# Kernel tuning notes

Hardware: AMD Instinct MI355X
Metric: run time of the kernel (lower is better)

Reference implementation:

```python
import jax, jax.numpy as jnp
import numpy as np

B = 131072
N = 19  # num_features, fixed by the hard-coded 19x19 correlation matrix


def _make_corr():
    corr = np.eye(N, dtype=np.float32)
    for i, j, v in [(0, 1, 0.9088), (2, 3, 0.7964), (2, 4, 0.6972),
                    (2, 9, -0.6945), (4, 9, -0.6679)]:
        corr[i, j] = corr[j, i] = v
    return jnp.asarray(corr)


def setup_inputs() -> dict:
    key = jax.random.key(0)
    ks = jax.random.split(key, 9)
    bound = 1.0 / np.sqrt(N)  # torch nn.Linear default init range

    def linear_params(k):
        kw, kb = jax.random.split(k)
        W = jax.random.uniform(kw, (N, N), jnp.float32, -bound, bound)
        b = jax.random.uniform(kb, (N,), jnp.float32, -bound, bound)
        return W, b

    Wq, bq = linear_params(ks[0])
    Wk, bk = linear_params(ks[1])
    Wv, bv = linear_params(ks[2])
    Wo, bo = linear_params(ks[3])
    features = jax.random.normal(ks[4], (B, N), jnp.float32)
    return {
        "features": features,
        "Wq": Wq, "bq": bq,
        "Wk": Wk, "bk": bk,
        "Wv": Wv, "bv": bv,
        "Wo": Wo, "bo": bo,
        "corr": _make_corr(),
        "temperature": jnp.array(1.0, jnp.float32),
    }


def reference(features, Wq, bq, Wk, bk, Wv, bv, Wo, bo, corr, temperature):
    # Projections (torch Linear: x @ W.T + b)
    Q = features @ Wq.T + bq  # [B, N]
    K = features @ Wk.T + bk  # [B, N]
    V = features @ Wv.T + bv  # [B, N]

    # Outer-product scores: bmm(Q[:, :, None], K[:, None, :]) -> [B, N, N]
    scores = Q[:, :, None] * K[:, None, :]

    # correlation_weight = (corr @ K.T).T = K @ corr.T ; mean over features -> [B]
    cw_mean = (K @ corr.T).mean(axis=-1)
    scores = scores * cw_mean[:, None, None]

    attention = jax.nn.softmax(scores / temperature, axis=-1)  # [B, N, N]

    # Elementwise combine (attention * V broadcast over the query axis)
    attended = attention * V[:, None, :]  # [B, N, N]

    output = attended @ Wo.T + bo  # [B, N, N]

    # Residual: features broadcast over the query axis
    return features[:, None, :] + output  # [B, N, N]
```

## Files before the change

kernel.cpp:

```cpp
#include <hip/hip_runtime.h>

#define B_TOTAL 131072
#define N 19
#define BB 13
#define ROWS (BB * N)
#define NPAD 20
#define OUT_PER_G (BB * N * N)

__global__ void cga_prep(const float* __restrict__ corr, float* __restrict__ c) {
    int t = threadIdx.x;
    if (t < N) {
        float s = 0.f;
#pragma unroll
        for (int i = 0; i < N; ++i) s += corr[i * N + t];
        c[t] = s * (1.0f / N);
    }
}

__global__ void __launch_bounds__(256) cga_kernel(
    const float* __restrict__ feats,
    const float* __restrict__ Wq, const float* __restrict__ bq,
    const float* __restrict__ Wk, const float* __restrict__ bk,
    const float* __restrict__ Wv, const float* __restrict__ bv,
    const float* __restrict__ Wo, const float* __restrict__ bo,
    const float* __restrict__ temp,
    const float* __restrict__ c,
    float* __restrict__ out)
{
    __shared__ __align__(16) float feat_s[BB * NPAD];
    __shared__ __align__(16) float k_s[BB * NPAD];
    __shared__ __align__(16) float v_s[BB * NPAD];
    __shared__ __align__(16) float out_s[OUT_PER_G];

    const int t = threadIdx.x;
    const int bl = t / N;
    const int i  = t - bl * N;
    const bool active = (t < ROWS);

    float wq[N], wk[N], wv[N];
    float bqv = 0.f, bkv = 0.f, bvv = 0.f;
    if (active) {
#pragma unroll
        for (int j = 0; j < N; ++j) {
            wq[j] = Wq[i * N + j];
            wk[j] = Wk[i * N + j];
            wv[j] = Wv[i * N + j];
        }
        bqv = bq[i]; bkv = bk[i]; bvv = bv[i];
    }
    const float invT = 1.0f / temp[0];

    const int G = (B_TOTAL + BB - 1) / BB;
    for (int g = blockIdx.x; g < G; g += gridDim.x) {
        const int b0 = g * BB;

        if (t < ROWS) {
            int gidx = b0 * N + t;
            float v = (gidx < B_TOTAL * N) ? feats[gidx] : 0.f;
            feat_s[(t / N) * NPAD + (t % N)] = v;
        }
        __syncthreads();

        float f[NPAD];
        float q_i = 0.f, k_i = 0.f, v_i = 0.f;
        if (active) {
            const float4* fp = (const float4*)(&feat_s[bl * NPAD]);
#pragma unroll
            for (int c4 = 0; c4 < 5; ++c4) {
                float4 x = fp[c4];
                f[c4*4+0] = x.x; f[c4*4+1] = x.y; f[c4*4+2] = x.z; f[c4*4+3] = x.w;
            }
            q_i = bqv; k_i = bkv; v_i = bvv;
#pragma unroll
            for (int j = 0; j < N; ++j) {
                q_i = fmaf(f[j], wq[j], q_i);
                k_i = fmaf(f[j], wk[j], k_i);
                v_i = fmaf(f[j], wv[j], v_i);
            }
            k_s[bl * NPAD + i] = k_i;
            v_s[bl * NPAD + i] = v_i;
        }
        __syncthreads();

        if (active) {
            float K[NPAD], V[NPAD];
            const float4* kp = (const float4*)(&k_s[bl * NPAD]);
            const float4* vp = (const float4*)(&v_s[bl * NPAD]);
#pragma unroll
            for (int c4 = 0; c4 < 5; ++c4) {
                float4 x = kp[c4];
                K[c4*4+0] = x.x; K[c4*4+1] = x.y; K[c4*4+2] = x.z; K[c4*4+3] = x.w;
                float4 y = vp[c4];
                V[c4*4+0] = y.x; V[c4*4+1] = y.y; V[c4*4+2] = y.z; V[c4*4+3] = y.w;
            }
            float cw = 0.f;
#pragma unroll
            for (int j = 0; j < N; ++j) cw = fmaf(c[j], K[j], cw);
            const float a = q_i * cw * invT;

            float s[N];
            float m = -1e30f;
#pragma unroll
            for (int j = 0; j < N; ++j) { s[j] = a * K[j]; m = fmaxf(m, s[j]); }
            float z = 0.f;
            float qv[N];
#pragma unroll
            for (int j = 0; j < N; ++j) {
                float e = __expf(s[j] - m);
                qv[j] = e * V[j];
                z += e;
            }
            const float invZ = 1.0f / z;

            const int obase = t * N;
#pragma unroll
            for (int k = 0; k < N; ++k) {
                float acc = 0.f;
#pragma unroll
                for (int j = 0; j < N; ++j) acc = fmaf(qv[j], Wo[k * N + j], acc);
                out_s[obase + k] = f[k] + bo[k] + acc * invZ;
            }
        }
        __syncthreads();

        const int outbase = b0 * (N * N);
#pragma unroll
        for (int r = 0; r < (OUT_PER_G + 255) / 256; ++r) {
            int idx = r * 256 + t;
            int go = outbase + idx;
            if (idx < OUT_PER_G && go < B_TOTAL * N * N)
                out[go] = out_s[idx];
        }
        __syncthreads();
    }
}

extern "C" void kernel_launch(void* const* d_in, const int* in_sizes, int n_in,
                              void* d_out, int out_size, void* d_ws, size_t ws_size,
                              hipStream_t stream) {
    const float* feats = (const float*)d_in[0];
    const float* Wq    = (const float*)d_in[1];
    const float* bq    = (const float*)d_in[2];
    const float* Wk    = (const float*)d_in[3];
    const float* bk    = (const float*)d_in[4];
    const float* Wv    = (const float*)d_in[5];
    const float* bv    = (const float*)d_in[6];
    const float* Wo    = (const float*)d_in[7];
    const float* bo    = (const float*)d_in[8];
    const float* corr  = (const float*)d_in[9];
    const float* temp  = (const float*)d_in[10];
    float* out = (float*)d_out;
    float* c   = (float*)d_ws;

    cga_prep<<<1, 64, 0, stream>>>(corr, c);
    cga_kernel<<<1024, 256, 0, stream>>>(feats, Wq, bq, Wk, bk, Wv, bv, Wo, bo,
                                         temp, c, out);
}
```

Measured before the change: 265.9 us.

## Replace persistent grid-stride loop with one block per group and fuse prep kernel

The persistent 1024-block grid-stride loop becomes a grid with one block per 13-sample group, and launch bounds now request 4 blocks per SM. The separate corr column-mean prep kernel is folded into each block, which now computes the column means into shared memory. Weights are read per use from global/cache instead of being held in registers across iterations. The aim is to remove a kernel launch, cut register pressure so occupancy rises, and let the hardware schedule groups to hide latency. In exchange every block redoes the corr reduction and reloads the weights.

Result: faster. 244.3 us (-8.1%).

```diff
diff --git a/kernel.cpp b/kernel.cpp
--- a/kernel.cpp
+++ b/kernel.cpp
@@ -6,132 +6,111 @@
 #define ROWS (BB * N)
 #define NPAD 20
 #define OUT_PER_G (BB * N * N)
+#define NBLOCKS ((B_TOTAL + BB - 1) / BB)
 
-__global__ void cga_prep(const float* __restrict__ corr, float* __restrict__ c) {
-    int t = threadIdx.x;
-    if (t < N) {
-        float s = 0.f;
-#pragma unroll
-        for (int i = 0; i < N; ++i) s += corr[i * N + t];
-        c[t] = s * (1.0f / N);
-    }
-}
-
-__global__ void __launch_bounds__(256) cga_kernel(
+__global__ void __launch_bounds__(256, 4) cga_kernel(
     const float* __restrict__ feats,
     const float* __restrict__ Wq, const float* __restrict__ bq,
     const float* __restrict__ Wk, const float* __restrict__ bk,
     const float* __restrict__ Wv, const float* __restrict__ bv,
     const float* __restrict__ Wo, const float* __restrict__ bo,
+    const float* __restrict__ corr,
     const float* __restrict__ temp,
-    const float* __restrict__ c,
     float* __restrict__ out)
 {
     __shared__ __align__(16) float feat_s[BB * NPAD];
     __shared__ __align__(16) float k_s[BB * NPAD];
     __shared__ __align__(16) float v_s[BB * NPAD];
+    __shared__ __align__(16) float c_s[NPAD];
     __shared__ __align__(16) float out_s[OUT_PER_G];
 
-    const int t = threadIdx.x;
+    const int t  = threadIdx.x;
+    const int b0 = blockIdx.x * BB;
     const int bl = t / N;
     const int i  = t - bl * N;
     const bool active = (t < ROWS);
 
-    float wq[N], wk[N], wv[N];
-    float bqv = 0.f, bkv = 0.f, bvv = 0.f;
     if (active) {
+        int gidx = b0 * N + t;
+        feat_s[bl * NPAD + i] = (gidx < B_TOTAL * N) ? feats[gidx] : 0.f;
+    }
+    if (t < N) {
+        float s = 0.f;
+#pragma unroll
+        for (int r = 0; r < N; ++r) s += corr[r * N + t];
+        c_s[t] = s * (1.0f / N);
+    }
+    const float invT = 1.0f / temp[0];
+    __syncthreads();
+
+    float f[NPAD];
+    float q_i = 0.f, k_i = 0.f, v_i = 0.f;
+    if (active) {
+        const float4* fp = (const float4*)(&feat_s[bl * NPAD]);
+#pragma unroll
+        for (int c4 = 0; c4 < 5; ++c4) {
+            float4 x = fp[c4];
+            f[c4*4+0] = x.x; f[c4*4+1] = x.y; f[c4*4+2] = x.z; f[c4*4+3] = x.w;
+        }
+        q_i = bq[i]; k_i = bk[i]; v_i = bv[i];
 #pragma unroll
         for (int j = 0; j < N; ++j) {
-            wq[j] = Wq[i * N + j];
-            wk[j] = Wk[i * N + j];
-            wv[j] = Wv[i * N + j];
+            q_i = fmaf(f[j], Wq[i * N + j], q_i);
+            k_i = fmaf(f[j], Wk[i * N + j], k_i);
+            v_i = fmaf(f[j], Wv[i * N + j], v_i);
         }
-        bqv = bq[i]; bkv = bk[i]; bvv = bv[i];
+        k_s[bl * NPAD + i] = k_i;
+        v_s[bl * NPAD + i] = v_i;
     }
-    const float invT = 1.0f / temp[0];
+    __syncthreads();
 
-    const int G = (B_TOTAL + BB - 1) / BB;
-    for (int g = blockIdx.x; g < G; g += gridDim.x) {
-        const int b0 = g * BB;
+    if (active) {
+        float K[NPAD], V[NPAD];
+        const float4* kp = (const float4*)(&k_s[bl * NPAD]);
+        const float4* vp = (const float4*)(&v_s[bl * NPAD]);
+#pragma unroll
+        for (int c4 = 0; c4 < 5; ++c4) {
+            float4 x = kp[c4];
+            K[c4*4+0] = x.x; K[c4*4+1] = x.y; K[c4*4+2] = x.z; K[c4*4+3] = x.w;
+            float4 y = vp[c4];
+            V[c4*4+0] = y.x; V[c4*4+1] = y.y; V[c4*4+2] = y.z; V[c4*4+3] = y.w;
+        }
+        float cw = 0.f;
+#pragma unroll
+        for (int j = 0; j < N; ++j) cw = fmaf(c_s[j], K[j], cw);
+        const float a = q_i * cw * invT;
 
-        if (t < ROWS) {
-            int gidx = b0 * N + t;
-            float v = (gidx < B_TOTAL * N) ? feats[gidx] : 0.f;
-            feat_s[(t / N) * NPAD + (t % N)] = v;
+        float m = -1e30f;
+#pragma unroll
+        for (int j = 0; j < N; ++j) m = fmaxf(m, a * K[j]);
+        float z = 0.f;
+        float p[N];
+#pragma unroll
+        for (int j = 0; j < N; ++j) {
+            float e = __expf(fmaf(a, K[j], -m));
+            p[j] = e * V[j];
+            z += e;
         }
-        __syncthreads();
+        const float invZ = 1.0f / z;
 
-        float f[NPAD];
-        float q_i = 0.f, k_i = 0.f, v_i = 0.f;
-        if (active) {
-            const float4* fp = (const float4*)(&feat_s[bl * NPAD]);
+        const int obase = t * N;
 #pragma unroll
-            for (int c4 = 0; c4 < 5; ++c4) {
-                float4 x = fp[c4];
-                f[c4*4+0] = x.x; f[c4*4+1] = x.y; f[c4*4+2] = x.z; f[c4*4+3] = x.w;
-            }
-            q_i = bqv; k_i = bkv; v_i = bvv;
+        for (int k = 0; k < N; ++k) {
+            float acc = 0.f;
 #pragma unroll
-            for (int j = 0; j < N; ++j) {
-                q_i = fmaf(f[j], wq[j], q_i);
-                k_i = fmaf(f[j], wk[j], k_i);
-                v_i = fmaf(f[j], wv[j], v_i);
-            }
-            k_s[bl * NPAD + i] = k_i;
-            v_s[bl * NPAD + i] = v_i;
+            for (int j = 0; j < N; ++j) acc = fmaf(p[j], Wo[k * N + j], acc);
+            out_s[obase + k] = f[k] + bo[k] + acc * invZ;
         }
-        __syncthreads();
+    }
+    __syncthreads();
 
-        if (active) {
-            float K[NPAD], V[NPAD];
-            const float4* kp = (const float4*)(&k_s[bl * NPAD]);
-            const float4* vp = (const float4*)(&v_s[bl * NPAD]);
+    const int outbase = b0 * (N * N);
 #pragma unroll
-            for (int c4 = 0; c4 < 5; ++c4) {
-                float4 x = kp[c4];
-                K[c4*4+0] = x.x; K[c4*4+1] = x.y; K[c4*4+2] = x.z; K[c4*4+3] = x.w;
-                float4 y = vp[c4];
-                V[c4*4+0] = y.x; V[c4*4+1] = y.y; V[c4*4+2] = y.z; V[c4*4+3] = y.w;
-            }
-            float cw = 0.f;
-#pragma unroll
-            for (int j = 0; j < N; ++j) cw = fmaf(c[j], K[j], cw);
-            const float a = q_i * cw * invT;
-
-            float s[N];
-            float m = -1e30f;
-#pragma unroll
-            for (int j = 0; j < N; ++j) { s[j] = a * K[j]; m = fmaxf(m, s[j]); }
-            float z = 0.f;
-            float qv[N];
-#pragma unroll
-            for (int j = 0; j < N; ++j) {
-                float e = __expf(s[j] - m);
-                qv[j] = e * V[j];
-                z += e;
-            }
-            const float invZ = 1.0f / z;
-
-            const int obase = t * N;
-#pragma unroll
-            for (int k = 0; k < N; ++k) {
-                float acc = 0.f;
-#pragma unroll
-                for (int j = 0; j < N; ++j) acc = fmaf(qv[j], Wo[k * N + j], acc);
-                out_s[obase + k] = f[k] + bo[k] + acc * invZ;
-            }
-        }
-        __syncthreads();
-
-        const int outbase = b0 * (N * N);
-#pragma unroll
-        for (int r = 0; r < (OUT_PER_G + 255) / 256; ++r) {
-            int idx = r * 256 + t;
-            int go = outbase + idx;
-            if (idx < OUT_PER_G && go < B_TOTAL * N * N)
-                out[go] = out_s[idx];
-        }
-        __syncthreads();
+    for (int r = 0; r < (OUT_PER_G + 255) / 256; ++r) {
+        int idx = r * 256 + t;
+        int go  = outbase + idx;
+        if (idx < OUT_PER_G && go < B_TOTAL * N * N)
+            out[go] = out_s[idx];
     }
 }
 
@@ -150,9 +129,7 @@
     const float* corr  = (const float*)d_in[9];
     const float* temp  = (const float*)d_in[10];
     float* out = (float*)d_out;
-    float* c   = (float*)d_ws;
 
-    cga_prep<<<1, 64, 0, stream>>>(corr, c);
-    cga_kernel<<<1024, 256, 0, stream>>>(feats, Wq, bq, Wk, bk, Wv, bv, Wo, bo,
-                                         temp, c, out);
+    cga_kernel<<<NBLOCKS, 256, 0, stream>>>(feats, Wq, bq, Wk, bk, Wv, bv,
+                                            Wo, bo, corr, temp, out);
 }
```
